# Kernel optimization log

Measured on AMD Instinct MI355X. Metric: run time of the kernel, lower is better.

## Reference

```python
import jax, jax.numpy as jnp
import numpy as np

B, S, D = 2, 512, 128      # batch, seq_len, d_att
DG, NG = 64, 2             # d_group, n_group = D // DG


def setup_inputs() -> dict:
    key = jax.random.key(0)
    ks = jax.random.split(key, 12)
    def w(k, shape, scale):
        return jax.random.normal(k, shape, dtype=jnp.float32) * scale
    proj_scale = 1.0 / D                      # xavier_uniform-ish std / sqrt(d_att)
    mlp1 = (2.0 / (DG + DG)) ** 0.5
    mlp2 = (2.0 / (DG + 16)) ** 0.5
    mlp3 = (2.0 / (16 + 1)) ** 0.5
    return {
        "x": w(ks[0], (B, S, D), 1.0),
        "positional_adding_bias": w(ks[1], (1, NG, 1, S, S), 1.0),
        "positional_multiplying_bias": jax.random.uniform(ks[2], (1, NG, 1, S, S), dtype=jnp.float32),
        "Wq": w(ks[3], (D, D), proj_scale),
        "Wk": w(ks[4], (D, D), proj_scale),
        "Wv": w(ks[5], (D, D), proj_scale),
        "W1": w(ks[6], (DG, DG), mlp1), "b1": jnp.zeros((DG,), jnp.float32),
        "W2": w(ks[7], (DG, 16), mlp2), "b2": jnp.zeros((16,), jnp.float32),
        "W3": w(ks[8], (16, 1), mlp3),  "b3": jnp.zeros((1,), jnp.float32),
    }


def reference(x, positional_adding_bias, positional_multiplying_bias,
              Wq, Wk, Wv, W1, b1, W2, b2, W3, b3):
    Q = x @ Wq   # [B,S,D]
    K = x @ Wk
    V = x @ Wv
    # pairwise Q-K differences, grouped: [B,S,S,NG,DG] (d_att split as n_group,d_group)
    diff = (Q[:, :, None, :] - K[:, None, :, :]).reshape(B, S, S, NG, DG)
    # per-group scoring MLP (Linear->ReLU x3, final width 1)
    h = jax.nn.relu(diff @ W1 + b1)
    h = jax.nn.relu(h @ W2 + b2)
    a = jax.nn.relu(h @ W3 + b3)                 # [B,S,S,NG,1]
    a = jnp.transpose(a, (0, 3, 4, 1, 2))        # [B,NG,1,S,S]
    a = a * positional_multiplying_bias + positional_adding_bias
    a = jax.nn.softmax(a, axis=-1)[:, :, 0]      # [B,NG,S,S], softmax over keys
    # NOTE: original reshapes V as (d_group, n_group) — faithful reproduction
    Vr = V.reshape(B, S, DG, NG)                 # [B,S,DG,NG]
    out = jnp.einsum('bisk,bkji->bsji', a, Vr)   # [B,S,DG,NG]
    return out.reshape(B, S, D)
```

## Files before the change

### kernel.cpp

```cpp
#include <hip/hip_runtime.h>

#define BQ 2
#define SQ 512
#define DQ 128
#define DGQ 64
#define NGQ 2

typedef float float2v __attribute__((ext_vector_type(2)));


__global__ __launch_bounds__(256) void proj_kernel(
    const float* __restrict__ x,
    const float* __restrict__ Wq, const float* __restrict__ Wk,
    const float* __restrict__ Wv,
    const float* __restrict__ W1, const float* __restrict__ b1,
    float* __restrict__ QW1, float* __restrict__ KW1, float* __restrict__ Vp)
{
    const int t = threadIdx.x;
    const int row = blockIdx.x;
    __shared__ float xs[DQ];
    __shared__ float part[3][2][DQ];
    __shared__ float qs[DQ], ks[DQ];

    if (t < DQ) xs[t] = x[(size_t)row * DQ + t];
    __syncthreads();

    const int f = t & 127, h = t >> 7;
    float aq = 0.f, ak = 0.f, av = 0.f;
    const int d0 = h * 64;
    #pragma unroll 8
    for (int d = 0; d < 64; ++d) {
        const float xv = xs[d0 + d];
        const size_t o = (size_t)(d0 + d) * DQ + f;
        aq = fmaf(xv, Wq[o], aq);
        ak = fmaf(xv, Wk[o], ak);
        av = fmaf(xv, Wv[o], av);
    }
    part[0][h][f] = aq; part[1][h][f] = ak; part[2][h][f] = av;
    __syncthreads();

    if (t < DQ) {
        qs[t] = part[0][0][t] + part[0][1][t];
        const float v = part[2][0][t] + part[2][1][t];
        Vp[((size_t)row * NGQ + (t & 1)) * DGQ + (t >> 1)] = v;
    } else {
        const int f2 = t - DQ;
        ks[f2] = part[1][0][f2] + part[1][1][f2];
    }
    __syncthreads();

    const int fb = t & 127, side = t >> 7;
    const int g = fb >> 6, c = fb & 63;
    const float* src = side ? ks : qs;
    float acc = side ? 0.f : b1[c];
    #pragma unroll 8
    for (int e = 0; e < 64; ++e)
        acc = fmaf(src[g * 64 + e], W1[e * DGQ + c], acc);
    (side ? KW1 : QW1)[(size_t)row * DQ + fb] = acc;
}

__global__ __launch_bounds__(512) void attn_kernel(
    const float* __restrict__ QW1, const float* __restrict__ KW1,
    const float* __restrict__ Vp,
    const float* __restrict__ W2, const float* __restrict__ b2,
    const float* __restrict__ W3, const float* __restrict__ b3,
    const float* __restrict__ pos_add, const float* __restrict__ pos_mul,
    float* __restrict__ out)
{
    const int t = threadIdx.x;
    const int ipair = blockIdx.x & 255;
    const int g = (blockIdx.x >> 8) & 1;
    const int b = blockIdx.x >> 9;
    const int i0 = ipair * 2;

    __shared__ __align__(16) float qsl[2][DGQ];
    __shared__ __align__(8)  float sc[SQ * 2];
    __shared__ float redm[2][8], reds[2][8];
    __shared__ float avs[2][8][DGQ];

    if (t < 2 * DGQ) {
        const int qq = t >> 6, e = t & 63;
        qsl[qq][e] = QW1[((size_t)(b * SQ + i0 + qq)) * DQ + g * DGQ + e];
    }
    const size_t bo0 = ((size_t)g * SQ + i0) * SQ + t;
    const float pm0 = pos_mul[bo0],      pa0 = pos_add[bo0];
    const float pm1 = pos_mul[bo0 + SQ], pa1 = pos_add[bo0 + SQ];
    __syncthreads();

    const float4* krow = reinterpret_cast<const float4*>(
        KW1 + ((size_t)(b * SQ + t)) * DQ + g * DGQ);
    const float4* qv0 = reinterpret_cast<const float4*>(&qsl[0][0]);
    const float4* qv1 = reinterpret_cast<const float4*>(&qsl[1][0]);
    const float2v* b2v = reinterpret_cast<const float2v*>(b2);
    const float2v zero2 = {0.f, 0.f};

    float2v acc0[8], acc1[8];
    #pragma unroll
    for (int o = 0; o < 8; ++o) { acc0[o] = b2v[o]; acc1[o] = b2v[o]; }

    float4 kva = krow[0], kvb = krow[1];
    #pragma unroll
    for (int grp = 0; grp < 8; ++grp) {
        float4 nka, nkb;
        if (grp < 7) { nka = krow[grp * 2 + 2]; nkb = krow[grp * 2 + 3]; }
        #pragma unroll
        for (int u = 0; u < 2; ++u) {
            const int c4 = grp * 2 + u;
            const float4 kv = u ? kvb : kva;
            const float4 qa = qv0[c4], qb = qv1[c4];
            const float2v k01 = {kv.x, kv.y}, k23 = {kv.z, kv.w};
            const float2v ha01 = __builtin_elementwise_max(
                float2v{qa.x, qa.y} - k01, zero2);
            const float2v ha23 = __builtin_elementwise_max(
                float2v{qa.z, qa.w} - k23, zero2);
            const float2v hb01 = __builtin_elementwise_max(
                float2v{qb.x, qb.y} - k01, zero2);
            const float2v hb23 = __builtin_elementwise_max(
                float2v{qb.z, qb.w} - k23, zero2);
            const float2v* w2r = reinterpret_cast<const float2v*>(W2 + c4 * 64);
            #pragma unroll
            for (int o = 0; o < 8; ++o) {
                const float2v w0 = w2r[o],      w1 = w2r[8 + o];
                const float2v w2_ = w2r[16 + o], w3_ = w2r[24 + o];
                acc0[o] += ha01.x * w0;  acc0[o] += ha01.y * w1;
                acc0[o] += ha23.x * w2_; acc0[o] += ha23.y * w3_;
                acc1[o] += hb01.x * w0;  acc1[o] += hb01.y * w1;
                acc1[o] += hb23.x * w2_; acc1[o] += hb23.y * w3_;
            }
        }
        kva = nka; kvb = nkb;
    }
    float a0 = b3[0], a1 = b3[0];
    #pragma unroll
    for (int o = 0; o < 8; ++o) {
        a0 = fmaf(fmaxf(acc0[o].x, 0.f), W3[2 * o], a0);
        a0 = fmaf(fmaxf(acc0[o].y, 0.f), W3[2 * o + 1], a0);
        a1 = fmaf(fmaxf(acc1[o].x, 0.f), W3[2 * o], a1);
        a1 = fmaf(fmaxf(acc1[o].y, 0.f), W3[2 * o + 1], a1);
    }
    const float logit0 = fmaf(fmaxf(a0, 0.f), pm0, pa0);
    const float logit1 = fmaf(fmaxf(a1, 0.f), pm1, pa1);

    float m0 = logit0, m1 = logit1;
    #pragma unroll
    for (int off = 32; off > 0; off >>= 1) {
        m0 = fmaxf(m0, __shfl_xor(m0, off));
        m1 = fmaxf(m1, __shfl_xor(m1, off));
    }
    const int wave = t >> 6;
    if ((t & 63) == 0) { redm[0][wave] = m0; redm[1][wave] = m1; }
    __syncthreads();
    float M0 = redm[0][0], M1 = redm[1][0];
    #pragma unroll
    for (int w = 1; w < 8; ++w) {
        M0 = fmaxf(M0, redm[0][w]); M1 = fmaxf(M1, redm[1][w]);
    }
    const float e0 = __expf(logit0 - M0);
    const float e1 = __expf(logit1 - M1);
    *reinterpret_cast<float2v*>(&sc[t * 2]) = float2v{e0, e1};
    float s0 = e0, s1 = e1;
    #pragma unroll
    for (int off = 32; off > 0; off >>= 1) {
        s0 += __shfl_xor(s0, off);
        s1 += __shfl_xor(s1, off);
    }
    if ((t & 63) == 0) { reds[0][wave] = s0; reds[1][wave] = s1; }
    __syncthreads();
    float S0 = 0.f, S1 = 0.f;
    #pragma unroll
    for (int w = 0; w < 8; ++w) { S0 += reds[0][w]; S1 += reds[1][w]; }
    const float inv0 = 1.f / S0, inv1 = 1.f / S1;

    const int dim = t & 63, q = t >> 6;
    const float* vbase = Vp + (((size_t)(b * SQ + q * 64)) * NGQ + g) * DGQ + dim;
    float2v accv = {0.f, 0.f};
    #pragma unroll 16
    for (int k = 0; k < 64; ++k) {
        const float v = vbase[(size_t)k * (NGQ * DGQ)];
        const float2v sv = *reinterpret_cast<const float2v*>(&sc[(q * 64 + k) * 2]);
        accv += v * sv;
    }
    avs[0][q][dim] = accv.x;
    avs[1][q][dim] = accv.y;
    __syncthreads();
    if (t < 2 * DGQ) {
        const int qq = t >> 6, d = t & 63;
        float sum = 0.f;
        #pragma unroll
        for (int w = 0; w < 8; ++w) sum += avs[qq][w][d];
        out[((size_t)(b * SQ + i0 + qq)) * DQ + d * NGQ + g] =
            sum * (qq ? inv1 : inv0);
    }
}

extern "C" void kernel_launch(void* const* d_in, const int* in_sizes, int n_in,
                              void* d_out, int out_size, void* d_ws, size_t ws_size,
                              hipStream_t stream) {
    const float* x       = (const float*)d_in[0];
    const float* pos_add = (const float*)d_in[1];
    const float* pos_mul = (const float*)d_in[2];
    const float* Wq      = (const float*)d_in[3];
    const float* Wk      = (const float*)d_in[4];
    const float* Wv      = (const float*)d_in[5];
    const float* W1      = (const float*)d_in[6];
    const float* b1      = (const float*)d_in[7];
    const float* W2      = (const float*)d_in[8];
    const float* b2      = (const float*)d_in[9];
    const float* W3      = (const float*)d_in[10];
    const float* b3      = (const float*)d_in[11];
    float* out = (float*)d_out;

    float* ws  = (float*)d_ws;
    float* QW1 = ws;
    float* KW1 = ws + 131072;
    float* Vp  = ws + 262144;

    proj_kernel<<<BQ * SQ, 256, 0, stream>>>(x, Wq, Wk, Wv, W1, b1,
                                             QW1, KW1, Vp);
    attn_kernel<<<BQ * NGQ * SQ / 2, 512, 0, stream>>>(QW1, KW1, Vp, W2, b2,
                                                       W3, b3, pos_add, pos_mul,
                                                       out);
}
```

Measured before the change: 119.0 us.

## Process four query rows per attention block to reuse K and W2 loads

The attention kernel now handles four query rows per block instead of two, halving the grid. Each thread's K row and each W2 load is reused across four MLP accumulator sets, and the softmax and V reduction are carried out for four rows at once. This cuts redundant K/W2 traffic and per-block overhead. In exchange, register pressure roughly doubles for the accumulators (64 floats), with launch bounds set to keep occupancy, and there are fewer blocks to spread across CUs.

```diff
diff --git a/kernel.cpp b/kernel.cpp
--- a/kernel.cpp
+++ b/kernel.cpp
@@ -59,7 +59,7 @@
     (side ? KW1 : QW1)[(size_t)row * DQ + fb] = acc;
 }
 
-__global__ __launch_bounds__(512) void attn_kernel(
+__global__ __launch_bounds__(512, 4) void attn_kernel(
     const float* __restrict__ QW1, const float* __restrict__ KW1,
     const float* __restrict__ Vp,
     const float* __restrict__ W2, const float* __restrict__ b2,
@@ -68,35 +68,40 @@
     float* __restrict__ out)
 {
     const int t = threadIdx.x;
-    const int ipair = blockIdx.x & 255;
-    const int g = (blockIdx.x >> 8) & 1;
-    const int b = blockIdx.x >> 9;
-    const int i0 = ipair * 2;
-
-    __shared__ __align__(16) float qsl[2][DGQ];
-    __shared__ __align__(8)  float sc[SQ * 2];
-    __shared__ float redm[2][8], reds[2][8];
-    __shared__ float avs[2][8][DGQ];
-
-    if (t < 2 * DGQ) {
+    const int itile = blockIdx.x & 127;
+    const int g = (blockIdx.x >> 7) & 1;
+    const int b = blockIdx.x >> 8;
+    const int i0 = itile * 4;
+    const int lane = t & 63, wv = t >> 6;
+
+    __shared__ __align__(16) float qsl[4][DGQ];
+    __shared__ __align__(16) float sc4[SQ][4];
+    __shared__ float redm[4][8], reds[4][8];
+    __shared__ float avs[4][8][DGQ];
+
+    if (t < 4 * DGQ) {
         const int qq = t >> 6, e = t & 63;
         qsl[qq][e] = QW1[((size_t)(b * SQ + i0 + qq)) * DQ + g * DGQ + e];
     }
-    const size_t bo0 = ((size_t)g * SQ + i0) * SQ + t;
-    const float pm0 = pos_mul[bo0],      pa0 = pos_add[bo0];
-    const float pm1 = pos_mul[bo0 + SQ], pa1 = pos_add[bo0 + SQ];
+    float pmv[4], pav[4];
+    #pragma unroll
+    for (int qq = 0; qq < 4; ++qq) {
+        const size_t bo = ((size_t)g * SQ + i0 + qq) * SQ + t;
+        pmv[qq] = pos_mul[bo];
+        pav[qq] = pos_add[bo];
+    }
     __syncthreads();
 
     const float4* krow = reinterpret_cast<const float4*>(
         KW1 + ((size_t)(b * SQ + t)) * DQ + g * DGQ);
-    const float4* qv0 = reinterpret_cast<const float4*>(&qsl[0][0]);
-    const float4* qv1 = reinterpret_cast<const float4*>(&qsl[1][0]);
     const float2v* b2v = reinterpret_cast<const float2v*>(b2);
     const float2v zero2 = {0.f, 0.f};
 
-    float2v acc0[8], acc1[8];
-    #pragma unroll
-    for (int o = 0; o < 8; ++o) { acc0[o] = b2v[o]; acc1[o] = b2v[o]; }
+    float2v acc[4][8];
+    #pragma unroll
+    for (int qq = 0; qq < 4; ++qq)
+        #pragma unroll
+        for (int o = 0; o < 8; ++o) acc[qq][o] = b2v[o];
 
     float4 kva = krow[0], kvb = krow[1];
     #pragma unroll
@@ -107,89 +112,101 @@
         for (int u = 0; u < 2; ++u) {
             const int c4 = grp * 2 + u;
             const float4 kv = u ? kvb : kva;
-            const float4 qa = qv0[c4], qb = qv1[c4];
             const float2v k01 = {kv.x, kv.y}, k23 = {kv.z, kv.w};
-            const float2v ha01 = __builtin_elementwise_max(
-                float2v{qa.x, qa.y} - k01, zero2);
-            const float2v ha23 = __builtin_elementwise_max(
-                float2v{qa.z, qa.w} - k23, zero2);
-            const float2v hb01 = __builtin_elementwise_max(
-                float2v{qb.x, qb.y} - k01, zero2);
-            const float2v hb23 = __builtin_elementwise_max(
-                float2v{qb.z, qb.w} - k23, zero2);
+            float2v h01[4], h23[4];
+            #pragma unroll
+            for (int qq = 0; qq < 4; ++qq) {
+                const float4 qa = reinterpret_cast<const float4*>(
+                    &qsl[qq][0])[c4];
+                h01[qq] = __builtin_elementwise_max(
+                    float2v{qa.x, qa.y} - k01, zero2);
+                h23[qq] = __builtin_elementwise_max(
+                    float2v{qa.z, qa.w} - k23, zero2);
+            }
             const float2v* w2r = reinterpret_cast<const float2v*>(W2 + c4 * 64);
             #pragma unroll
             for (int o = 0; o < 8; ++o) {
                 const float2v w0 = w2r[o],      w1 = w2r[8 + o];
                 const float2v w2_ = w2r[16 + o], w3_ = w2r[24 + o];
-                acc0[o] += ha01.x * w0;  acc0[o] += ha01.y * w1;
-                acc0[o] += ha23.x * w2_; acc0[o] += ha23.y * w3_;
-                acc1[o] += hb01.x * w0;  acc1[o] += hb01.y * w1;
-                acc1[o] += hb23.x * w2_; acc1[o] += hb23.y * w3_;
+                #pragma unroll
+                for (int qq = 0; qq < 4; ++qq) {
+                    acc[qq][o] += h01[qq].x * w0;
+                    acc[qq][o] += h01[qq].y * w1;
+                    acc[qq][o] += h23[qq].x * w2_;
+                    acc[qq][o] += h23[qq].y * w3_;
+                }
             }
         }
         kva = nka; kvb = nkb;
     }
-    float a0 = b3[0], a1 = b3[0];
-    #pragma unroll
-    for (int o = 0; o < 8; ++o) {
-        a0 = fmaf(fmaxf(acc0[o].x, 0.f), W3[2 * o], a0);
-        a0 = fmaf(fmaxf(acc0[o].y, 0.f), W3[2 * o + 1], a0);
-        a1 = fmaf(fmaxf(acc1[o].x, 0.f), W3[2 * o], a1);
-        a1 = fmaf(fmaxf(acc1[o].y, 0.f), W3[2 * o + 1], a1);
-    }
-    const float logit0 = fmaf(fmaxf(a0, 0.f), pm0, pa0);
-    const float logit1 = fmaf(fmaxf(a1, 0.f), pm1, pa1);
-
-    float m0 = logit0, m1 = logit1;
-    #pragma unroll
-    for (int off = 32; off > 0; off >>= 1) {
-        m0 = fmaxf(m0, __shfl_xor(m0, off));
-        m1 = fmaxf(m1, __shfl_xor(m1, off));
-    }
-    const int wave = t >> 6;
-    if ((t & 63) == 0) { redm[0][wave] = m0; redm[1][wave] = m1; }
-    __syncthreads();
-    float M0 = redm[0][0], M1 = redm[1][0];
-    #pragma unroll
-    for (int w = 1; w < 8; ++w) {
-        M0 = fmaxf(M0, redm[0][w]); M1 = fmaxf(M1, redm[1][w]);
-    }
-    const float e0 = __expf(logit0 - M0);
-    const float e1 = __expf(logit1 - M1);
-    *reinterpret_cast<float2v*>(&sc[t * 2]) = float2v{e0, e1};
-    float s0 = e0, s1 = e1;
-    #pragma unroll
-    for (int off = 32; off > 0; off >>= 1) {
-        s0 += __shfl_xor(s0, off);
-        s1 += __shfl_xor(s1, off);
-    }
-    if ((t & 63) == 0) { reds[0][wave] = s0; reds[1][wave] = s1; }
-    __syncthreads();
-    float S0 = 0.f, S1 = 0.f;
-    #pragma unroll
-    for (int w = 0; w < 8; ++w) { S0 += reds[0][w]; S1 += reds[1][w]; }
-    const float inv0 = 1.f / S0, inv1 = 1.f / S1;
-
-    const int dim = t & 63, q = t >> 6;
-    const float* vbase = Vp + (((size_t)(b * SQ + q * 64)) * NGQ + g) * DGQ + dim;
-    float2v accv = {0.f, 0.f};
-    #pragma unroll 16
+
+    float logit[4];
+    #pragma unroll
+    for (int qq = 0; qq < 4; ++qq) {
+        float a = b3[0];
+        #pragma unroll
+        for (int o = 0; o < 8; ++o) {
+            a = fmaf(fmaxf(acc[qq][o].x, 0.f), W3[2 * o], a);
+            a = fmaf(fmaxf(acc[qq][o].y, 0.f), W3[2 * o + 1], a);
+        }
+        logit[qq] = fmaf(fmaxf(a, 0.f), pmv[qq], pav[qq]);
+    }
+
+    float m[4] = {logit[0], logit[1], logit[2], logit[3]};
+    #pragma unroll
+    for (int off = 32; off > 0; off >>= 1)
+        #pragma unroll
+        for (int qq = 0; qq < 4; ++qq) m[qq] = fmaxf(m[qq], __shfl_xor(m[qq], off));
+    if (lane == 0)
+        #pragma unroll
+        for (int qq = 0; qq < 4; ++qq) redm[qq][wv] = m[qq];
+    __syncthreads();
+    float e[4], s[4];
+    #pragma unroll
+    for (int qq = 0; qq < 4; ++qq) {
+        float M = redm[qq][0];
+        #pragma unroll
+        for (int w = 1; w < 8; ++w) M = fmaxf(M, redm[qq][w]);
+        e[qq] = __expf(logit[qq] - M);
+        s[qq] = e[qq];
+    }
+    *reinterpret_cast<float4*>(&sc4[t][0]) =
+        float4{e[0], e[1], e[2], e[3]};
+    #pragma unroll
+    for (int off = 32; off > 0; off >>= 1)
+        #pragma unroll
+        for (int qq = 0; qq < 4; ++qq) s[qq] += __shfl_xor(s[qq], off);
+    if (lane == 0)
+        #pragma unroll
+        for (int qq = 0; qq < 4; ++qq) reds[qq][wv] = s[qq];
+    __syncthreads();
+    float inv[4];
+    #pragma unroll
+    for (int qq = 0; qq < 4; ++qq) {
+        float S = 0.f;
+        #pragma unroll
+        for (int w = 0; w < 8; ++w) S += reds[qq][w];
+        inv[qq] = 1.f / S;
+    }
+
+    const float* vbase = Vp + (((size_t)(b * SQ + wv * 64)) * NGQ + g) * DGQ + lane;
+    float2v av01 = {0.f, 0.f}, av23 = {0.f, 0.f};
+    #pragma unroll 8
     for (int k = 0; k < 64; ++k) {
         const float v = vbase[(size_t)k * (NGQ * DGQ)];
-        const float2v sv = *reinterpret_cast<const float2v*>(&sc[(q * 64 + k) * 2]);
-        accv += v * sv;
-    }
-    avs[0][q][dim] = accv.x;
-    avs[1][q][dim] = accv.y;
-    __syncthreads();
-    if (t < 2 * DGQ) {
+        const float4 sv = *reinterpret_cast<const float4*>(&sc4[wv * 64 + k][0]);
+        av01 += v * float2v{sv.x, sv.y};
+        av23 += v * float2v{sv.z, sv.w};
+    }
+    avs[0][wv][lane] = av01.x; avs[1][wv][lane] = av01.y;
+    avs[2][wv][lane] = av23.x; avs[3][wv][lane] = av23.y;
+    __syncthreads();
+    if (t < 4 * DGQ) {
         const int qq = t >> 6, d = t & 63;
         float sum = 0.f;
         #pragma unroll
         for (int w = 0; w < 8; ++w) sum += avs[qq][w][d];
-        out[((size_t)(b * SQ + i0 + qq)) * DQ + d * NGQ + g] =
-            sum * (qq ? inv1 : inv0);
+        out[((size_t)(b * SQ + i0 + qq)) * DQ + d * NGQ + g] = sum * inv[qq];
     }
 }
 
@@ -217,7 +234,7 @@
 
     proj_kernel<<<BQ * SQ, 256, 0, stream>>>(x, Wq, Wk, Wv, W1, b1,
                                              QW1, KW1, Vp);
-    attn_kernel<<<BQ * NGQ * SQ / 2, 512, 0, stream>>>(QW1, KW1, Vp, W2, b2,
+    attn_kernel<<<BQ * NGQ * SQ / 4, 512, 0, stream>>>(QW1, KW1, Vp, W2, b2,
                                                        W3, b3, pos_add, pos_mul,
                                                        out);
 }
```

Measured after the change: 120.6 us. No clear change (+1.3%).
